# Performance work log

Hardware: AMD Instinct MI355X
Metric: run time of the kernel (lower is better)

The kernel has to match this reference:

```python
import jax, jax.numpy as jnp
from jax import lax
import numpy as np

B, N, M, K, NS, C = 8, 8192, 512, 6, 16, 13  # batch, points, clusters, nc2p, nsample, classes
D = 64  # point feature dim

def _fps(xyz, m):
    """Furthest point sampling over one cloud [n,3] -> [m] int32 indices."""
    n = xyz.shape[0]
    def body(carry, _):
        dist, last = carry
        d = jnp.sum((xyz - xyz[last]) ** 2, axis=-1)
        dist = jnp.minimum(dist, d)
        return (dist, jnp.argmax(dist).astype(jnp.int32)), last
    (_, _), idxs = lax.scan(body, (jnp.full((n,), 1e10, xyz.dtype), jnp.int32(0)), None, length=m)
    return idxs

def _gather(src, idx):
    # src [B, S, d] (or [B, S]), idx [B, ...] -> [B, ..., d]
    return jax.vmap(lambda s, i: s[i])(src, idx)

def _scatter_weighted(idx, w, val, m):
    # idx [B,n,K] cluster ids, w [B,n,K] weights, val [B,n,d] -> weighted mean per cluster [B,m,d]
    def one(i_b, w_b, v_b):
        num = jnp.zeros((m, v_b.shape[-1]), v_b.dtype).at[i_b].add(w_b[..., None] * v_b[:, None, :])
        den = jnp.zeros((m,), w_b.dtype).at[i_b].add(w_b)
        return num / jnp.maximum(den, 1e-8)[:, None]
    return jax.vmap(one)(idx, w, val)

def _mlp2(x, W1, W2):
    return jax.nn.relu(jax.nn.relu(x @ W1) @ W2)

def _forward(pointcloud, clouds_knn, onehot_label, label,
             bb_Wk1, bb_Wk2, bb_Wg, head_W1, head_W2,
             slic_Wf1, slic_Wf2, slic_Wx1, slic_Wx2, slic_Wm1, slic_Wm2):
    xyz = pointcloud[..., :3]              # [B,N,3]
    fea = pointcloud[..., 3:]              # [B,N,3]
    # --- FPS + KNN cluster association (pointops.furthestsampling / knnquerycluster) ---
    cluster_idx = jax.vmap(lambda x: _fps(x, M))(xyz)            # [B,M]
    cluster_xyz = _gather(xyz, cluster_idx)                      # [B,M,3]
    d2 = jnp.sum((xyz[:, :, None, :] - cluster_xyz[:, None, :, :]) ** 2, axis=-1)  # [B,N,M]
    _, c2p_idx_abs = lax.top_k(-d2, K)                           # [B,N,K] cluster ids
    c2p_idx = _gather(cluster_idx, c2p_idx_abs)                  # [B,N,K] point ids of clusters
    # --- association matrix + per-cluster label histogram (pointops.assomatrixpluslabel) ---
    def build(i_b, lab_b):
        A = jnp.zeros((M, N), jnp.float32).at[i_b, jnp.arange(N)[:, None]].add(1.0)
        L = jnp.zeros((M, C), jnp.float32).at[i_b.reshape(-1), jnp.repeat(lab_b, K)].add(1.0)
        return A, A.sum(-1, keepdims=True), L
    asso_matrix, sp_nei_cnt, sp_lab = jax.vmap(build)(c2p_idx_abs, label)
    # --- backbone (LPE_stn): per-point local KNN branch (max-pool) + global feature branch ---
    hk = jnp.max(_mlp2(clouds_knn, bb_Wk1, bb_Wk2), axis=2)      # [B,N,64]
    hg = jax.nn.relu(fea @ bb_Wg)                                # [B,N,64]
    p_fea = hk + hg                                              # [B,N,64]
    out = jax.nn.relu(p_fea @ head_W1) @ head_W2                 # [B,N,C] semantic logits
    # --- init_fea: average associated point features per cluster ---
    sp_fea = jnp.einsum('bmn,bnd->bmd', asso_matrix, p_fea) / jnp.maximum(sp_nei_cnt, 1.0)
    sp_xyz = cluster_xyz
    fea_dist = None
    for l in range(4):
        fd = _gather(sp_fea, c2p_idx_abs) - p_fea[:, :, None, :]   # [B,N,K,64]
        xd = _gather(sp_xyz, c2p_idx_abs) - xyz[:, :, None, :]     # [B,N,K,3]
        wf = _mlp2(fd, slic_Wf1[l], slic_Wf2[l])                   # [B,N,K,16]
        wx = _mlp2(xd, slic_Wx1[l], slic_Wx2[l])                   # [B,N,K,16]
        pm = _mlp2(p_fea, slic_Wm1[l], slic_Wm2[l])                # [B,N,16]
        logits = jnp.sum(wf * wx * pm[:, :, None, :], axis=-1)    # [B,N,K]
        w = jax.nn.softmax(logits, axis=-1)
        sp_fea = _scatter_weighted(c2p_idx_abs, w, p_fea, M)
        sp_xyz = _scatter_weighted(c2p_idx_abs, w, xyz, M)
        fea_dist = w
    final_asso = fea_dist                                         # [B,N,K]
    # --- reconstruction branch ---
    p2sp_idx = jnp.argmax(final_asso, axis=2)                     # [B,N]
    sel = jnp.take_along_axis(c2p_idx_abs, p2sp_idx[..., None], 2)[..., 0]
    re_p_xyz = _gather(sp_xyz, sel)                               # [B,N,3]
    sp_label = _scatter_weighted(c2p_idx_abs, final_asso, onehot_label, M)  # [B,M,C]
    c2p_label = _gather(sp_label, c2p_idx_abs)                    # [B,N,K,C]
    re_p_label = jnp.sum(c2p_label * final_asso[..., None], axis=2)  # [B,N,C]
    sp_pseudo_lab = jnp.argmax(sp_lab, axis=2)                    # [B,M]
    sp_pseudo_lab_onehot = jax.nn.one_hot(sp_pseudo_lab, C, dtype=jnp.float32).transpose(0, 2, 1)
    return (final_asso, cluster_idx, c2p_idx, c2p_idx_abs, out, re_p_xyz, re_p_label,
            fea_dist, p_fea, sp_label.transpose(0, 2, 1), sp_pseudo_lab, sp_pseudo_lab_onehot)

def setup_inputs() -> dict:
    key = jax.random.key(0)
    ks = jax.random.split(key, 20)
    s = lambda k, shp, sc: (jax.random.normal(k, shp, jnp.float32) * sc)
    return {
        'pointcloud': jax.random.normal(ks[0], (B, N, 6), jnp.float32),
        'clouds_knn': jax.random.normal(ks[1], (B, N, NS, 2), jnp.float32),
        'onehot_label': jax.random.uniform(ks[2], (B, N, C), jnp.float32),
        'label': jax.random.randint(ks[3], (B, N), 0, C, jnp.int32),
        'bb_Wk1': s(ks[4], (2, 32), 0.5), 'bb_Wk2': s(ks[5], (32, D), 0.15),
        'bb_Wg': s(ks[6], (3, D), 0.4),
        'head_W1': s(ks[7], (D, D), 0.12), 'head_W2': s(ks[8], (D, C), 0.12),
        'slic_Wf1': s(ks[9], (4, D, 16), 0.12), 'slic_Wf2': s(ks[10], (4, 16, 16), 0.25),
        'slic_Wx1': s(ks[11], (4, 3, 16), 0.5), 'slic_Wx2': s(ks[12], (4, 16, 16), 0.25),
        'slic_Wm1': s(ks[13], (4, D, 16), 0.12), 'slic_Wm2': s(ks[14], (4, 16, 16), 0.25),
    }

def reference(pointcloud, clouds_knn, onehot_label, label,
              bb_Wk1, bb_Wk2, bb_Wg, head_W1, head_W2,
              slic_Wf1, slic_Wf2, slic_Wx1, slic_Wx2, slic_Wm1, slic_Wm2):
    return _forward(pointcloud, clouds_knn, onehot_label, label,
                    bb_Wk1, bb_Wk2, bb_Wg, head_W1, head_W2,
                    slic_Wf1, slic_Wf2, slic_Wx1, slic_Wx2, slic_Wm1, slic_Wm2)
```

## Files before the change

### kernel.cpp

```cpp
#include <hip/hip_runtime.h>

#define BB 8
#define NN 8192
#define MM 512
#define KK 6
#define NSAMP 16
#define CC 13
#define DD 64

#define O_ASSO   0u
#define O_CIDX   393216u
#define O_C2P    397312u
#define O_C2PA   790528u
#define O_OUT    1183744u
#define O_RPXYZ  2035712u
#define O_RPLAB  2232320u
#define O_FDIST  3084288u
#define O_PFEA   3477504u
#define O_SPLABT 7671808u
#define O_PSLAB  7725056u
#define O_PSOH   7729152u

__device__ __forceinline__ unsigned long long dpp_max_u64(unsigned long long k) {
  int lo = (int)(unsigned)(k & 0xFFFFFFFFull);
  int hi = (int)(unsigned)(k >> 32);
#define DPP_STEP(ctrl)                                                         \
  {                                                                            \
    int nlo = __builtin_amdgcn_update_dpp(0, lo, ctrl, 0xf, 0xf, true);        \
    int nhi = __builtin_amdgcn_update_dpp(0, hi, ctrl, 0xf, 0xf, true);        \
    unsigned long long nk =                                                    \
        ((unsigned long long)(unsigned)nhi << 32) | (unsigned)nlo;             \
    unsigned long long ck =                                                    \
        ((unsigned long long)(unsigned)hi << 32) | (unsigned)lo;               \
    if (nk > ck) { lo = nlo; hi = nhi; }                                       \
  }
  DPP_STEP(0x111)
  DPP_STEP(0x112)
  DPP_STEP(0x114)
  DPP_STEP(0x118)
  DPP_STEP(0x142)
  DPP_STEP(0x143)
#undef DPP_STEP
  return ((unsigned long long)(unsigned)hi << 32) | (unsigned)lo;
}

__global__ __launch_bounds__(512, 1) void k_fps(const float* __restrict__ pc,
                                                int* __restrict__ cidx,
                                                float* __restrict__ cxyz,
                                                float* __restrict__ out) {
  __shared__ float sx[NN], sy[NN], sz[NN];
  __shared__ unsigned long long s_best[2][8];
  __shared__ int   s_pidx[MM];
  __shared__ float s_px[MM], s_py[MM], s_pz[MM];
  const int t = threadIdx.x;
  const int b = blockIdx.x;
  const float* xb = pc + (size_t)b * NN * 6;
  float px[16], py[16], pz[16], dist[16];
#pragma unroll
  for (int j = 0; j < 16; ++j) {
    int p = t + j * 512;
    float X = xb[(size_t)p*6+0], Y = xb[(size_t)p*6+1], Z = xb[(size_t)p*6+2];
    px[j] = X; py[j] = Y; pz[j] = Z; dist[j] = 1e10f;
    sx[p] = X; sy[p] = Y; sz[p] = Z;
  }
  __syncthreads();
  float lx = sx[0], ly = sy[0], lz = sz[0];
  if (t == 0) { s_pidx[0] = 0; s_px[0] = lx; s_py[0] = ly; s_pz[0] = lz; }
  const int lane = t & 63, wave = t >> 6;
  for (int step = 1; step < MM; ++step) {
    float bv = -1.0f; int bp = 0;
#pragma unroll
    for (int j = 0; j < 16; ++j) {
      float dx = px[j]-lx, dy = py[j]-ly, dz = pz[j]-lz;
      float d = __fadd_rn(__fadd_rn(__fmul_rn(dx,dx), __fmul_rn(dy,dy)), __fmul_rn(dz,dz));
      float nd = fminf(dist[j], d);
      dist[j] = nd;
      if (nd > bv) { bv = nd; bp = t + j*512; }
    }
    unsigned long long key = ((unsigned long long)__float_as_uint(bv) << 32)
                           | (unsigned)(0xFFFFFFFFu - (unsigned)bp);
    key = dpp_max_u64(key);
    if (lane == 63) s_best[step & 1][wave] = key;
    __syncthreads();
    const ulonglong2* sb = (const ulonglong2*)s_best[step & 1];
    ulonglong2 q0 = sb[0], q1 = sb[1], q2 = sb[2], q3 = sb[3];
    unsigned long long kk = q0.x;
    if (q0.y > kk) kk = q0.y;
    if (q1.x > kk) kk = q1.x;
    if (q1.y > kk) kk = q1.y;
    if (q2.x > kk) kk = q2.x;
    if (q2.y > kk) kk = q2.y;
    if (q3.x > kk) kk = q3.x;
    if (q3.y > kk) kk = q3.y;
    int p = (int)(0xFFFFFFFFu - (unsigned)(kk & 0xFFFFFFFFull));
    lx = sx[p]; ly = sy[p]; lz = sz[p];
    if (t == 0) {
      s_pidx[step] = p;
      s_px[step] = lx; s_py[step] = ly; s_pz[step] = lz;
    }
  }
  __syncthreads();
  if (t < MM) {
    int p = s_pidx[t];
    cidx[b*MM + t] = p;
    out[O_CIDX + b*MM + t] = (float)p;
    cxyz[((size_t)b*MM + t)*3+0] = s_px[t];
    cxyz[((size_t)b*MM + t)*3+1] = s_py[t];
    cxyz[((size_t)b*MM + t)*3+2] = s_pz[t];
  }
}

__attribute__((amdgpu_waves_per_eu(1, 2)))
__global__ __launch_bounds__(256) void k_pfea(const float* __restrict__ pc,
                                              const float* __restrict__ knn,
                                              const float* __restrict__ Wk1,
                                              const float* __restrict__ Wk2,
                                              const float* __restrict__ Wg,
                                              const float* __restrict__ hW1,
                                              const float* __restrict__ hW2,
                                              float* __restrict__ xyz,
                                              float* __restrict__ out) {
  int i = blockIdx.x * 256 + threadIdx.x;
  const float2* pr = (const float2*)(pc + (size_t)i*6);
  float2 r0 = pr[0], r1 = pr[1], r2 = pr[2];
  float* xo = xyz + (size_t)i*3;
  xo[0] = r0.x; xo[1] = r0.y; xo[2] = r1.x;
  float acc[DD];
#pragma unroll
  for (int d = 0; d < DD; ++d) acc[d] = -3.4e38f;
  const float* kp = knn + (size_t)i * NSAMP * 2;
  for (int s = 0; s < NSAMP; ++s) {
    float u = kp[s*2+0], v2 = kp[s*2+1];
    float h1[32];
#pragma unroll
    for (int j = 0; j < 32; ++j) h1[j] = fmaxf(u*Wk1[j] + v2*Wk1[32+j], 0.f);
#pragma unroll
    for (int d = 0; d < DD; ++d) {
      float tt = 0.f;
#pragma unroll
      for (int j = 0; j < 32; ++j) tt += h1[j]*Wk2[j*DD+d];
      acc[d] = fmaxf(acc[d], tt);
    }
  }
  float f0 = r1.y, f1 = r2.x, f2 = r2.y;
#pragma unroll
  for (int d = 0; d < DD; ++d) {
    float hg = fmaxf(f0*Wg[d] + f1*Wg[DD+d] + f2*Wg[2*DD+d], 0.f);
    acc[d] = fmaxf(acc[d], 0.f) + hg;
    out[O_PFEA + (size_t)i*DD + d] = acc[d];
  }
  float o[CC];
#pragma unroll
  for (int c = 0; c < CC; ++c) o[c] = 0.f;
  for (int d = 0; d < DD; ++d) {
    float t1 = 0.f;
#pragma unroll
    for (int j = 0; j < DD; ++j) t1 += acc[j]*hW1[j*DD+d];
    t1 = fmaxf(t1, 0.f);
#pragma unroll
    for (int c = 0; c < CC; ++c) o[c] += t1*hW2[d*CC+c];
  }
#pragma unroll
  for (int c = 0; c < CC; ++c) out[O_OUT + (size_t)i*CC + c] = o[c];
}

__global__ __launch_bounds__(256) void k_knn(const float* __restrict__ xyz,
                      const float* __restrict__ cxyz,
                      const int* __restrict__ cidx, int* __restrict__ c2p,
                      float* __restrict__ out) {
  __shared__ float4 sc[MM];
  int i = blockIdx.x * 256 + threadIdx.x;
  int b = i >> 13;
  for (int m = threadIdx.x; m < MM; m += 256) {
    sc[m] = make_float4(cxyz[((size_t)b*MM+m)*3+0], cxyz[((size_t)b*MM+m)*3+1],
                        cxyz[((size_t)b*MM+m)*3+2], 0.f);
  }
  __syncthreads();
  float x = xyz[(size_t)i*3+0], y = xyz[(size_t)i*3+1], z = xyz[(size_t)i*3+2];
  float dv[KK]; int di[KK];
#pragma unroll
  for (int j = 0; j < KK; ++j) { dv[j] = 3.4e38f; di[j] = 0; }
  for (int m = 0; m < MM; ++m) {
    float4 c = sc[m];
    float dx = x - c.x, dy = y - c.y, dz = z - c.z;
    float d = __fadd_rn(__fadd_rn(__fmul_rn(dx,dx), __fmul_rn(dy,dy)), __fmul_rn(dz,dz));
    if (d < dv[KK-1]) {
      float v = d; int vi = m; bool ins = false;
#pragma unroll
      for (int j = 0; j < KK; ++j) {
        bool doit = ins || (v < dv[j]);
        float tv = doit ? dv[j] : v; int ti = doit ? di[j] : vi;
        if (doit) { dv[j] = v; di[j] = vi; }
        v = tv; vi = ti; ins = doit;
      }
    }
  }
#pragma unroll
  for (int k = 0; k < KK; ++k) {
    c2p[(size_t)i*KK+k] = di[k];
    out[O_C2PA + (size_t)i*KK + k] = (float)di[k];
    out[O_C2P  + (size_t)i*KK + k] = (float)cidx[b*MM + di[k]];
  }
}

__global__ __launch_bounds__(1024) void k_csr(const int* __restrict__ c2p,
                                              const int* __restrict__ label,
                                              int* __restrict__ cnt_g,
                                              int* __restrict__ offs_g,
                                              int* __restrict__ entries,
                                              float* __restrict__ out) {
  __shared__ int s_cnt[MM];
  __shared__ int s_off[MM];
  __shared__ int s_cur[MM];
  __shared__ int s_lab[MM*CC];
  int b = blockIdx.x, t = threadIdx.x;
  for (int i = t; i < MM; i += 1024) s_cnt[i] = 0;
  for (int i = t; i < MM*CC; i += 1024) s_lab[i] = 0;
  __syncthreads();
  const int* cb = c2p + (size_t)b*NN*KK;
  const int* lb = label + (size_t)b*NN;
  for (int n = t; n < NN; n += 1024) {
    int lab = lb[n];
#pragma unroll
    for (int k = 0; k < KK; ++k) {
      int m = cb[(size_t)n*KK+k];
      atomicAdd(&s_cnt[m], 1);
      atomicAdd(&s_lab[m*CC+lab], 1);
    }
  }
  __syncthreads();
  if (t < MM) s_off[t] = s_cnt[t];
  __syncthreads();
  for (int off = 1; off < MM; off <<= 1) {
    int v = 0;
    if (t < MM && t >= off) v = s_off[t-off];
    __syncthreads();
    if (t < MM && t >= off) s_off[t] += v;
    __syncthreads();
  }
  if (t < MM) {
    int ex = (t == 0) ? 0 : s_off[t-1];
    s_cur[t] = ex;
    offs_g[b*MM+t] = ex;
    cnt_g[b*MM+t] = s_cnt[t];
    int best = 0, bv = s_lab[t*CC];
#pragma unroll
    for (int c = 1; c < CC; ++c) { int v = s_lab[t*CC+c]; if (v > bv) { bv = v; best = c; } }
    out[O_PSLAB + b*MM + t] = (float)best;
#pragma unroll
    for (int c = 0; c < CC; ++c)
      out[O_PSOH + ((size_t)b*CC + c)*MM + t] = (c == best) ? 1.0f : 0.0f;
  }
  __syncthreads();
  for (int n = t; n < NN; n += 1024) {
#pragma unroll
    for (int k = 0; k < KK; ++k) {
      int m = cb[(size_t)n*KK+k];
      int pos = atomicAdd(&s_cur[m], 1);
      entries[(size_t)b*NN*KK + pos] = n*KK + k;
    }
  }
}

__global__ __launch_bounds__(256, 1) void k_scat(const float* __restrict__ pfea,
                          const float* __restrict__ xyz,
                          const float* __restrict__ w,
                          const float* __restrict__ cxyz,
                          const float* __restrict__ onehot,
                          const int* __restrict__ entries, const int* __restrict__ offs,
                          const int* __restrict__ cnt,
                          const float* __restrict__ Wf1n,
                          float* __restrict__ sp_fea, float* __restrict__ sp_xyz,
                          float* __restrict__ sp_label, float* __restrict__ smeta,
                          float* __restrict__ out) {
  int bm = blockIdx.x;
  int b = bm >> 9, m = bm & (MM-1);
  int t = threadIdx.x;
  int wv = t >> 6, lane = t & 63;
  int base = b*NN*KK;
  int st = offs[bm], n_e = cnt[bm];
  __shared__ int   s_ent[1024];
  __shared__ float s_w[1024];
  __shared__ float s_f[4][DD], s_x[4][4], s_l[4][16], s_d[4];
  __shared__ float s_sf[DD], s_part[16][17];
  float acc = 0.f, accx = 0.f, accl = 0.f, den = 0.f;
  for (int c0 = 0; c0 < n_e; c0 += 1024) {
    int cn = min(1024, n_e - c0);
    __syncthreads();
    for (int e = t; e < cn; e += 256) {
      int ee = entries[base + st + c0 + e];
      s_ent[e] = ee;
      s_w[e] = w ? w[(size_t)base + ee] : 1.0f;
    }
    __syncthreads();
    for (int e = wv; e < cn; e += 4) {
      int ee = s_ent[e]; float ww = s_w[e];
      int n = ee / KK;
      acc += ww * pfea[((size_t)b*NN+n)*DD + lane];
      if (lane < 3) accx += ww * xyz[((size_t)b*NN+n)*3 + lane];
      if (onehot && lane < CC) accl += ww * onehot[((size_t)b*NN+n)*CC + lane];
      den += ww;
    }
  }
  s_f[wv][lane] = acc;
  if (lane < 4)  s_x[wv][lane] = (lane < 3) ? accx : 0.f;
  if (lane < 16) s_l[wv][lane] = (lane < CC) ? accl : 0.f;
  if (lane == 0) s_d[wv] = den;
  __syncthreads();
  if (wv == 0) {
    float A  = s_f[0][lane] + s_f[1][lane] + s_f[2][lane] + s_f[3][lane];
    float Dn = s_d[0] + s_d[1] + s_d[2] + s_d[3];
    float dv = w ? fmaxf(Dn, 1e-8f) : fmaxf(Dn, 1.0f);
    float sfv = A / dv;
    sp_fea[(size_t)bm*DD + lane] = sfv;
    s_sf[lane] = sfv;
    if (lane < 3) {
      float X = w ? (s_x[0][lane]+s_x[1][lane]+s_x[2][lane]+s_x[3][lane]) / dv
                  : cxyz[bm*3+lane];
      sp_xyz[bm*3+lane] = X;
      if (Wf1n) smeta[bm*20 + 16 + lane] = X;
    }
    if (onehot && lane < CC) {
      float L = (s_l[0][lane]+s_l[1][lane]+s_l[2][lane]+s_l[3][lane]) / fmaxf(Dn, 1e-8f);
      sp_label[(size_t)bm*CC + lane] = L;
      out[O_SPLABT + ((size_t)b*CC + lane)*MM + m] = L;
    }
  }
  if (Wf1n) {
    __syncthreads();
    int c = t & 15, part = t >> 4;
    float pr = 0.f;
#pragma unroll
    for (int q = 0; q < 4; ++q)
      pr += s_sf[part*4+q] * Wf1n[(part*4+q)*16 + c];
    s_part[part][c] = pr;
    __syncthreads();
    if (t < 16) {
      float sm = 0.f;
#pragma unroll
      for (int q = 0; q < 16; ++q) sm += s_part[q][t];
      smeta[bm*20 + t] = sm;
    }
  }
}

__attribute__((amdgpu_waves_per_eu(1, 2)))
__global__ __launch_bounds__(256) void k_slicw(const float* __restrict__ pfea,
                        const float* __restrict__ xyz,
                        const float* __restrict__ smeta,
                        const int* __restrict__ c2p,
                        const float* __restrict__ Wf1, const float* __restrict__ Wf2,
                        const float* __restrict__ Wx1, const float* __restrict__ Wx2,
                        const float* __restrict__ Wm1, const float* __restrict__ Wm2,
                        float* __restrict__ wout, float* __restrict__ wout2) {
  int i = blockIdx.x*256 + threadIdx.x;
  int b = i >> 13;
  float pf[DD];
  const float4* pf4 = (const float4*)(pfea + (size_t)i*DD);
#pragma unroll
  for (int q = 0; q < DD/4; ++q) {
    float4 t = pf4[q];
    pf[q*4+0] = t.x; pf[q*4+1] = t.y; pf[q*4+2] = t.z; pf[q*4+3] = t.w;
  }
  float a[16];
#pragma unroll
  for (int c = 0; c < 16; ++c) a[c] = 0.f;
#pragma unroll
  for (int d = 0; d < DD; ++d) {
    float f = pf[d];
#pragma unroll
    for (int c = 0; c < 16; ++c) a[c] += f*Wm1[d*16+c];
  }
  float pm[16];
#pragma unroll
  for (int c2 = 0; c2 < 16; ++c2) {
    float t = 0.f;
#pragma unroll
    for (int c = 0; c < 16; ++c) t += fmaxf(a[c], 0.f)*Wm2[c*16+c2];
    pm[c2] = fmaxf(t, 0.f);
  }
  float pfd[16];
#pragma unroll
  for (int c = 0; c < 16; ++c) pfd[c] = 0.f;
#pragma unroll
  for (int d = 0; d < DD; ++d) {
    float f = pf[d];
#pragma unroll
    for (int c = 0; c < 16; ++c) pfd[c] += f*Wf1[d*16+c];
  }
  float x = xyz[(size_t)i*3+0], y = xyz[(size_t)i*3+1], z = xyz[(size_t)i*3+2];
  float lg[KK];
#pragma unroll 1
  for (int k = 0; k < KK; ++k) {
    int m = c2p[(size_t)i*KK+k];
    int bm = (b << 9) + m;
    const float4* mp = (const float4*)(smeta + (size_t)bm*20);
    float4 m0 = mp[0], m1 = mp[1], m2 = mp[2], m3 = mp[3], m4 = mp[4];
    float wa[16];
    wa[0]=m0.x-pfd[0];  wa[1]=m0.y-pfd[1];  wa[2]=m0.z-pfd[2];  wa[3]=m0.w-pfd[3];
    wa[4]=m1.x-pfd[4];  wa[5]=m1.y-pfd[5];  wa[6]=m1.z-pfd[6];  wa[7]=m1.w-pfd[7];
    wa[8]=m2.x-pfd[8];  wa[9]=m2.y-pfd[9];  wa[10]=m2.z-pfd[10]; wa[11]=m2.w-pfd[11];
    wa[12]=m3.x-pfd[12]; wa[13]=m3.y-pfd[13]; wa[14]=m3.z-pfd[14]; wa[15]=m3.w-pfd[15];
    float wf[16];
#pragma unroll
    for (int c2 = 0; c2 < 16; ++c2) {
      float t = 0.f;
#pragma unroll
      for (int c = 0; c < 16; ++c) t += fmaxf(wa[c], 0.f)*Wf2[c*16+c2];
      wf[c2] = fmaxf(t, 0.f);
    }
    float dx = m4.x - x, dy = m4.y - y, dz = m4.z - z;
    float ax[16];
#pragma unroll
    for (int c = 0; c < 16; ++c)
      ax[c] = fmaxf(dx*Wx1[c] + dy*Wx1[16+c] + dz*Wx1[32+c], 0.f);
    float lgk = 0.f;
#pragma unroll
    for (int c2 = 0; c2 < 16; ++c2) {
      float t = 0.f;
#pragma unroll
      for (int c = 0; c < 16; ++c) t += ax[c]*Wx2[c*16+c2];
      lgk += fmaxf(t, 0.f)*wf[c2]*pm[c2];
    }
    lg[k] = lgk;
  }
  float mx = lg[0];
#pragma unroll
  for (int k = 1; k < KK; ++k) mx = fmaxf(mx, lg[k]);
  float e[KK], s = 0.f;
#pragma unroll
  for (int k = 0; k < KK; ++k) { e[k] = expf(lg[k]-mx); s += e[k]; }
#pragma unroll
  for (int k = 0; k < KK; ++k) {
    float wv = e[k]/s;
    wout[(size_t)i*KK+k] = wv;
    if (wout2) wout2[(size_t)i*KK+k] = wv;
  }
}

__global__ __launch_bounds__(256) void k_final(const float* __restrict__ sp_xyz, const float* __restrict__ sp_label,
                        const int* __restrict__ c2p, float* __restrict__ out) {
  int i = blockIdx.x*256 + threadIdx.x;
  int b = i >> 13;
  float w[KK]; int id[KK];
#pragma unroll
  for (int k = 0; k < KK; ++k) {
    w[k] = out[O_ASSO + (size_t)i*KK+k];
    id[k] = c2p[(size_t)i*KK+k];
  }
  int best = 0; float bv = w[0];
#pragma unroll
  for (int k = 1; k < KK; ++k) if (w[k] > bv) { bv = w[k]; best = k; }
  int sel = id[best];
#pragma unroll
  for (int c = 0; c < 3; ++c)
    out[O_RPXYZ + (size_t)i*3+c] = sp_xyz[((size_t)b*MM+sel)*3+c];
  float acc[CC];
#pragma unroll
  for (int c = 0; c < CC; ++c) acc[c] = 0.f;
#pragma unroll
  for (int k = 0; k < KK; ++k) {
    const float* sl = sp_label + ((size_t)b*MM + id[k])*CC;
    float ww = w[k];
#pragma unroll
    for (int c = 0; c < CC; ++c) acc[c] += ww*sl[c];
  }
#pragma unroll
  for (int c = 0; c < CC; ++c) out[O_RPLAB + (size_t)i*CC+c] = acc[c];
}

extern "C" void kernel_launch(void* const* d_in, const int* in_sizes, int n_in,
                              void* d_out, int out_size, void* d_ws, size_t ws_size,
                              hipStream_t stream) {
  const float* pc     = (const float*)d_in[0];
  const float* knn    = (const float*)d_in[1];
  const float* onehot = (const float*)d_in[2];
  const int*   label  = (const int*)d_in[3];
  const float* Wk1    = (const float*)d_in[4];
  const float* Wk2    = (const float*)d_in[5];
  const float* Wg     = (const float*)d_in[6];
  const float* hW1    = (const float*)d_in[7];
  const float* hW2    = (const float*)d_in[8];
  const float* Wf1    = (const float*)d_in[9];
  const float* Wf2    = (const float*)d_in[10];
  const float* Wx1    = (const float*)d_in[11];
  const float* Wx2    = (const float*)d_in[12];
  const float* Wm1    = (const float*)d_in[13];
  const float* Wm2    = (const float*)d_in[14];
  float* out = (float*)d_out;

  float* wsf = (float*)d_ws;
  size_t o = 0;
  float* xyz     = wsf + o; o += (size_t)BB*NN*3;
  float* cxyz    = wsf + o; o += (size_t)BB*MM*3;
  int*   cidx    = (int*)(wsf + o); o += BB*MM;
  int*   c2p     = (int*)(wsf + o); o += (size_t)BB*NN*KK;
  int*   cnt     = (int*)(wsf + o); o += BB*MM;
  int*   offs    = (int*)(wsf + o); o += BB*MM;
  int*   entries = (int*)(wsf + o); o += (size_t)BB*NN*KK;
  float* sp_fea  = wsf + o; o += (size_t)BB*MM*DD;
  float* sp_xyz  = wsf + o; o += (size_t)BB*MM*3;
  float* sp_label= wsf + o; o += (size_t)BB*MM*CC;
  float* smeta   = wsf + o; o += (size_t)BB*MM*20;

  k_fps  <<<BB, 512, 0, stream>>>(pc, cidx, cxyz, out);
  k_pfea <<<BB*NN/256, 256, 0, stream>>>(pc, knn, Wk1, Wk2, Wg, hW1, hW2, xyz, out);
  k_knn  <<<BB*NN/256, 256, 0, stream>>>(xyz, cxyz, cidx, c2p, out);
  k_csr  <<<BB, 1024, 0, stream>>>(c2p, label, cnt, offs, entries, out);
  k_scat<<<BB*MM, 256, 0, stream>>>(out + O_PFEA, xyz, nullptr, cxyz, nullptr,
      entries, offs, cnt, Wf1 , sp_fea, sp_xyz, nullptr, smeta, out);
  for (int l = 0; l < 4; ++l) {
    k_slicw<<<BB*NN/256, 256, 0, stream>>>(out + O_PFEA, xyz, smeta, c2p,
        Wf1 + l*DD*16, Wf2 + l*256, Wx1 + l*48, Wx2 + l*256,
        Wm1 + l*DD*16, Wm2 + l*256,
        out + O_ASSO, (l == 3) ? (out + O_FDIST) : nullptr);
    k_scat<<<BB*MM, 256, 0, stream>>>(out + O_PFEA, xyz, out + O_ASSO, cxyz,
        (l == 3) ? onehot : nullptr, entries, offs, cnt,
        (l < 3) ? (Wf1 + (l+1)*DD*16) : nullptr,
        sp_fea, sp_xyz, sp_label, smeta, out);
  }
  k_final<<<BB*NN/256, 256, 0, stream>>>(sp_xyz, sp_label, c2p, out);
}
```

Before: 1.570 ms.

## Fuse FPS and point-feature kernels into one launch to overlap them

Merges the furthest-point-sampling kernel and the per-point feature MLP kernel into a single launch. The first 8 blocks run FPS and the rest compute point features, so the serial FPS loop runs alongside the parallel MLP work instead of before it. FPS now uses 256 threads with 32 points per thread and four independent argmax chains, which shortens the cross-wave reduction. Every block now reserves the large FPS shared-memory arrays, and waves_per_eu is forced to 1, which may lower occupancy for the MLP blocks. The longer per-thread FPS loop may also lengthen the critical path.

```diff
diff --git a/kernel.cpp b/kernel.cpp
--- a/kernel.cpp
+++ b/kernel.cpp
@@ -44,74 +44,8 @@
   return ((unsigned long long)(unsigned)hi << 32) | (unsigned)lo;
 }
 
-__global__ __launch_bounds__(512, 1) void k_fps(const float* __restrict__ pc,
-                                                int* __restrict__ cidx,
-                                                float* __restrict__ cxyz,
-                                                float* __restrict__ out) {
-  __shared__ float sx[NN], sy[NN], sz[NN];
-  __shared__ unsigned long long s_best[2][8];
-  __shared__ int   s_pidx[MM];
-  __shared__ float s_px[MM], s_py[MM], s_pz[MM];
-  const int t = threadIdx.x;
-  const int b = blockIdx.x;
-  const float* xb = pc + (size_t)b * NN * 6;
-  float px[16], py[16], pz[16], dist[16];
-#pragma unroll
-  for (int j = 0; j < 16; ++j) {
-    int p = t + j * 512;
-    float X = xb[(size_t)p*6+0], Y = xb[(size_t)p*6+1], Z = xb[(size_t)p*6+2];
-    px[j] = X; py[j] = Y; pz[j] = Z; dist[j] = 1e10f;
-    sx[p] = X; sy[p] = Y; sz[p] = Z;
-  }
-  __syncthreads();
-  float lx = sx[0], ly = sy[0], lz = sz[0];
-  if (t == 0) { s_pidx[0] = 0; s_px[0] = lx; s_py[0] = ly; s_pz[0] = lz; }
-  const int lane = t & 63, wave = t >> 6;
-  for (int step = 1; step < MM; ++step) {
-    float bv = -1.0f; int bp = 0;
-#pragma unroll
-    for (int j = 0; j < 16; ++j) {
-      float dx = px[j]-lx, dy = py[j]-ly, dz = pz[j]-lz;
-      float d = __fadd_rn(__fadd_rn(__fmul_rn(dx,dx), __fmul_rn(dy,dy)), __fmul_rn(dz,dz));
-      float nd = fminf(dist[j], d);
-      dist[j] = nd;
-      if (nd > bv) { bv = nd; bp = t + j*512; }
-    }
-    unsigned long long key = ((unsigned long long)__float_as_uint(bv) << 32)
-                           | (unsigned)(0xFFFFFFFFu - (unsigned)bp);
-    key = dpp_max_u64(key);
-    if (lane == 63) s_best[step & 1][wave] = key;
-    __syncthreads();
-    const ulonglong2* sb = (const ulonglong2*)s_best[step & 1];
-    ulonglong2 q0 = sb[0], q1 = sb[1], q2 = sb[2], q3 = sb[3];
-    unsigned long long kk = q0.x;
-    if (q0.y > kk) kk = q0.y;
-    if (q1.x > kk) kk = q1.x;
-    if (q1.y > kk) kk = q1.y;
-    if (q2.x > kk) kk = q2.x;
-    if (q2.y > kk) kk = q2.y;
-    if (q3.x > kk) kk = q3.x;
-    if (q3.y > kk) kk = q3.y;
-    int p = (int)(0xFFFFFFFFu - (unsigned)(kk & 0xFFFFFFFFull));
-    lx = sx[p]; ly = sy[p]; lz = sz[p];
-    if (t == 0) {
-      s_pidx[step] = p;
-      s_px[step] = lx; s_py[step] = ly; s_pz[step] = lz;
-    }
-  }
-  __syncthreads();
-  if (t < MM) {
-    int p = s_pidx[t];
-    cidx[b*MM + t] = p;
-    out[O_CIDX + b*MM + t] = (float)p;
-    cxyz[((size_t)b*MM + t)*3+0] = s_px[t];
-    cxyz[((size_t)b*MM + t)*3+1] = s_py[t];
-    cxyz[((size_t)b*MM + t)*3+2] = s_pz[t];
-  }
-}
-
-__attribute__((amdgpu_waves_per_eu(1, 2)))
-__global__ __launch_bounds__(256) void k_pfea(const float* __restrict__ pc,
+__attribute__((amdgpu_waves_per_eu(1, 1)))
+__global__ __launch_bounds__(256) void k_uber(const float* __restrict__ pc,
                                               const float* __restrict__ knn,
                                               const float* __restrict__ Wk1,
                                               const float* __restrict__ Wk2,
@@ -119,49 +53,123 @@
                                               const float* __restrict__ hW1,
                                               const float* __restrict__ hW2,
                                               float* __restrict__ xyz,
+                                              int* __restrict__ cidx,
+                                              float* __restrict__ cxyz,
                                               float* __restrict__ out) {
-  int i = blockIdx.x * 256 + threadIdx.x;
-  const float2* pr = (const float2*)(pc + (size_t)i*6);
-  float2 r0 = pr[0], r1 = pr[1], r2 = pr[2];
-  float* xo = xyz + (size_t)i*3;
-  xo[0] = r0.x; xo[1] = r0.y; xo[2] = r1.x;
-  float acc[DD];
-#pragma unroll
-  for (int d = 0; d < DD; ++d) acc[d] = -3.4e38f;
-  const float* kp = knn + (size_t)i * NSAMP * 2;
-  for (int s = 0; s < NSAMP; ++s) {
-    float u = kp[s*2+0], v2 = kp[s*2+1];
-    float h1[32];
-#pragma unroll
-    for (int j = 0; j < 32; ++j) h1[j] = fmaxf(u*Wk1[j] + v2*Wk1[32+j], 0.f);
+  __shared__ float sx[NN], sy[NN], sz[NN];
+  __shared__ unsigned long long s_best[2][4];
+  __shared__ int   s_pidx[MM];
+  __shared__ float s_px[MM], s_py[MM], s_pz[MM];
+  const int t = threadIdx.x;
+  if (blockIdx.x < 8) {
+    const int b = blockIdx.x;
+    const float* xb = pc + (size_t)b * NN * 6;
+    float px[32], py[32], pz[32], dist[32];
+#pragma unroll
+    for (int j = 0; j < 32; ++j) {
+      int p = t + j * 256;
+      float X = xb[(size_t)p*6+0], Y = xb[(size_t)p*6+1], Z = xb[(size_t)p*6+2];
+      px[j] = X; py[j] = Y; pz[j] = Z; dist[j] = 1e10f;
+      sx[p] = X; sy[p] = Y; sz[p] = Z;
+    }
+    __syncthreads();
+    float lx = sx[0], ly = sy[0], lz = sz[0];
+    if (t == 0) { s_pidx[0] = 0; s_px[0] = lx; s_py[0] = ly; s_pz[0] = lz; }
+    const int lane = t & 63, wave = t >> 6;
+    for (int step = 1; step < MM; ++step) {
+      float bv0 = -1.f, bv1 = -1.f, bv2 = -1.f, bv3 = -1.f;
+      int   bp0 = 0,    bp1 = 0,    bp2 = 0,    bp3 = 0;
+#define FPS_CHUNK(c, BV, BP)                                                   \
+      _Pragma("unroll")                                                        \
+      for (int j = 8*(c); j < 8*(c)+8; ++j) {                                  \
+        float dx = px[j]-lx, dy = py[j]-ly, dz = pz[j]-lz;                     \
+        float d = __fadd_rn(__fadd_rn(__fmul_rn(dx,dx), __fmul_rn(dy,dy)),     \
+                            __fmul_rn(dz,dz));                                 \
+        float nd = fminf(dist[j], d);                                          \
+        dist[j] = nd;                                                          \
+        if (nd > BV) { BV = nd; BP = t + j*256; }                              \
+      }
+      FPS_CHUNK(0, bv0, bp0)
+      FPS_CHUNK(1, bv1, bp1)
+      FPS_CHUNK(2, bv2, bp2)
+      FPS_CHUNK(3, bv3, bp3)
+#undef FPS_CHUNK
+      if (bv1 > bv0) { bv0 = bv1; bp0 = bp1; }
+      if (bv3 > bv2) { bv2 = bv3; bp2 = bp3; }
+      if (bv2 > bv0) { bv0 = bv2; bp0 = bp2; }
+      unsigned long long key = ((unsigned long long)__float_as_uint(bv0) << 32)
+                             | (unsigned)(0xFFFFFFFFu - (unsigned)bp0);
+      key = dpp_max_u64(key);
+      if (lane == 63) s_best[step & 1][wave] = key;
+      __syncthreads();
+      const ulonglong2* sb = (const ulonglong2*)s_best[step & 1];
+      ulonglong2 q0 = sb[0], q1 = sb[1];
+      unsigned long long kk = q0.x;
+      if (q0.y > kk) kk = q0.y;
+      if (q1.x > kk) kk = q1.x;
+      if (q1.y > kk) kk = q1.y;
+      int p = (int)(0xFFFFFFFFu - (unsigned)(kk & 0xFFFFFFFFull));
+      lx = sx[p]; ly = sy[p]; lz = sz[p];
+      if (t == 0) {
+        s_pidx[step] = p;
+        s_px[step] = lx; s_py[step] = ly; s_pz[step] = lz;
+      }
+    }
+    __syncthreads();
+#pragma unroll
+    for (int r = 0; r < 2; ++r) {
+      int m = t + r*256;
+      int p = s_pidx[m];
+      cidx[b*MM + m] = p;
+      out[O_CIDX + b*MM + m] = (float)p;
+      cxyz[((size_t)b*MM + m)*3+0] = s_px[m];
+      cxyz[((size_t)b*MM + m)*3+1] = s_py[m];
+      cxyz[((size_t)b*MM + m)*3+2] = s_pz[m];
+    }
+  } else {
+    int i = (blockIdx.x - 8) * 256 + t;
+    const float2* pr = (const float2*)(pc + (size_t)i*6);
+    float2 r0 = pr[0], r1 = pr[1], r2 = pr[2];
+    float* xo = xyz + (size_t)i*3;
+    xo[0] = r0.x; xo[1] = r0.y; xo[2] = r1.x;
+    float acc[DD];
+#pragma unroll
+    for (int d = 0; d < DD; ++d) acc[d] = -3.4e38f;
+    const float* kp = knn + (size_t)i * NSAMP * 2;
+    for (int s = 0; s < NSAMP; ++s) {
+      float u = kp[s*2+0], v2 = kp[s*2+1];
+      float h1[32];
+#pragma unroll
+      for (int j = 0; j < 32; ++j) h1[j] = fmaxf(u*Wk1[j] + v2*Wk1[32+j], 0.f);
+#pragma unroll
+      for (int d = 0; d < DD; ++d) {
+        float tt = 0.f;
+#pragma unroll
+        for (int j = 0; j < 32; ++j) tt += h1[j]*Wk2[j*DD+d];
+        acc[d] = fmaxf(acc[d], tt);
+      }
+    }
+    float f0 = r1.y, f1 = r2.x, f2 = r2.y;
 #pragma unroll
     for (int d = 0; d < DD; ++d) {
-      float tt = 0.f;
-#pragma unroll
-      for (int j = 0; j < 32; ++j) tt += h1[j]*Wk2[j*DD+d];
-      acc[d] = fmaxf(acc[d], tt);
-    }
-  }
-  float f0 = r1.y, f1 = r2.x, f2 = r2.y;
-#pragma unroll
-  for (int d = 0; d < DD; ++d) {
-    float hg = fmaxf(f0*Wg[d] + f1*Wg[DD+d] + f2*Wg[2*DD+d], 0.f);
-    acc[d] = fmaxf(acc[d], 0.f) + hg;
-    out[O_PFEA + (size_t)i*DD + d] = acc[d];
-  }
-  float o[CC];
-#pragma unroll
-  for (int c = 0; c < CC; ++c) o[c] = 0.f;
-  for (int d = 0; d < DD; ++d) {
-    float t1 = 0.f;
-#pragma unroll
-    for (int j = 0; j < DD; ++j) t1 += acc[j]*hW1[j*DD+d];
-    t1 = fmaxf(t1, 0.f);
-#pragma unroll
-    for (int c = 0; c < CC; ++c) o[c] += t1*hW2[d*CC+c];
-  }
-#pragma unroll
-  for (int c = 0; c < CC; ++c) out[O_OUT + (size_t)i*CC + c] = o[c];
+      float hg = fmaxf(f0*Wg[d] + f1*Wg[DD+d] + f2*Wg[2*DD+d], 0.f);
+      acc[d] = fmaxf(acc[d], 0.f) + hg;
+      out[O_PFEA + (size_t)i*DD + d] = acc[d];
+    }
+    float o[CC];
+#pragma unroll
+    for (int c = 0; c < CC; ++c) o[c] = 0.f;
+    for (int d = 0; d < DD; ++d) {
+      float t1 = 0.f;
+#pragma unroll
+      for (int j = 0; j < DD; ++j) t1 += acc[j]*hW1[j*DD+d];
+      t1 = fmaxf(t1, 0.f);
+#pragma unroll
+      for (int c = 0; c < CC; ++c) o[c] += t1*hW2[d*CC+c];
+    }
+#pragma unroll
+    for (int c = 0; c < CC; ++c) out[O_OUT + (size_t)i*CC + c] = o[c];
+  }
 }
 
 __global__ __launch_bounds__(256) void k_knn(const float* __restrict__ xyz,
@@ -503,8 +511,8 @@
   float* sp_label= wsf + o; o += (size_t)BB*MM*CC;
   float* smeta   = wsf + o; o += (size_t)BB*MM*20;
 
-  k_fps  <<<BB, 512, 0, stream>>>(pc, cidx, cxyz, out);
-  k_pfea <<<BB*NN/256, 256, 0, stream>>>(pc, knn, Wk1, Wk2, Wg, hW1, hW2, xyz, out);
+  k_uber <<<8 + BB*NN/256, 256, 0, stream>>>(pc, knn, Wk1, Wk2, Wg, hW1, hW2,
+                                             xyz, cidx, cxyz, out);
   k_knn  <<<BB*NN/256, 256, 0, stream>>>(xyz, cxyz, cidx, c2p, out);
   k_csr  <<<BB, 1024, 0, stream>>>(c2p, label, cnt, offs, entries, out);
   k_scat<<<BB*MM, 256, 0, stream>>>(out + O_PFEA, xyz, nullptr, cxyz, nullptr,
```

Measured after the change: 2.157 ms. 1.37x slower.
